# Kernel tuning notes

Hardware: AMD Instinct MI355X
Metric: run time of the kernel (lower is better)

## Reference

```python
import math
import jax, jax.numpy as jnp
import numpy as np

B, L, C, H = 2, 2048, 1024, 16
D = C // H


def new_gelu(x):
    return 0.5 * x * (1.0 + jnp.tanh(math.sqrt(2.0 / math.pi) * (x + 0.044715 * x ** 3)))


def layer_norm(x, w, b, eps=1e-5):
    mu = jnp.mean(x, axis=-1, keepdims=True)
    var = jnp.var(x, axis=-1, keepdims=True)
    return (x - mu) * jax.lax.rsqrt(var + eps) * w + b


def setup_inputs() -> dict:
    key = jax.random.key(0)
    ks = jax.random.split(key, 8)
    s = 0.02
    return {
        "x": jax.random.normal(ks[0], (B, L, C), dtype=jnp.float32),
        "ln1_w": jnp.ones((C,), jnp.float32),
        "ln1_b": jnp.zeros((C,), jnp.float32),
        "w_attn": jax.random.normal(ks[1], (C, 3 * C), dtype=jnp.float32) * s,
        "b_attn": jnp.zeros((3 * C,), jnp.float32),
        "w_proj": jax.random.normal(ks[2], (C, C), dtype=jnp.float32) * s,
        "b_proj": jnp.zeros((C,), jnp.float32),
        "ln2_w": jnp.ones((C,), jnp.float32),
        "ln2_b": jnp.zeros((C,), jnp.float32),
        "w_fc": jax.random.normal(ks[3], (C, 4 * C), dtype=jnp.float32) * s,
        "b_fc": jnp.zeros((4 * C,), jnp.float32),
        "w_fc2": jax.random.normal(ks[4], (4 * C, C), dtype=jnp.float32) * s,
        "b_fc2": jnp.zeros((C,), jnp.float32),
    }


def reference(x, ln1_w, ln1_b, w_attn, b_attn, w_proj, b_proj,
              ln2_w, ln2_b, w_fc, b_fc, w_fc2, b_fc2):
    # --- self-attention sublayer (pre-LN) ---
    h = layer_norm(x, ln1_w, ln1_b)
    qkv = h @ w_attn + b_attn                              # [B, L, 3C]
    q, k, v = jnp.split(qkv, 3, axis=-1)
    q = q.reshape(B, L, H, D)
    k = k.reshape(B, L, H, D)
    v = v.reshape(B, L, H, D)
    att = jnp.einsum("bqhd,bkhd->bhqk", q, k) * (1.0 / math.sqrt(D))
    causal = jnp.tril(jnp.ones((L, L), dtype=bool))
    att = jnp.where(causal[None, None], att, -jnp.inf)
    att = jax.nn.softmax(att, axis=-1)
    y = jnp.einsum("bhqk,bkhd->bqhd", att, v).reshape(B, L, C)
    y = y @ w_proj + b_proj
    x = x + y
    # --- MLP sublayer (pre-LN) ---
    h = layer_norm(x, ln2_w, ln2_b)
    h = new_gelu(h @ w_fc + b_fc)
    h = h @ w_fc2 + b_fc2
    return x + h
```

## Files before the change

### kernel.cpp

```cpp
#include <hip/hip_runtime.h>
#include <math.h>

#define B_ 2
#define L_ 2048
#define C_ 1024
#define H_ 16
#define M_ (B_*L_)

typedef short s16x8 __attribute__((ext_vector_type(8)));
typedef float f32x4 __attribute__((ext_vector_type(4)));

__device__ __forceinline__ unsigned short f2bf(float f) {
    unsigned int u = __float_as_uint(f);
    u += 0x7fffu + ((u >> 16) & 1u);
    return (unsigned short)(u >> 16);
}

__device__ __forceinline__ float fexp2(float x) {
#if __has_builtin(__builtin_amdgcn_exp2f)
    return __builtin_amdgcn_exp2f(x);
#else
    return exp2f(x);
#endif
}

__device__ __forceinline__ float frcp(float x) {
#if __has_builtin(__builtin_amdgcn_rcpf)
    return __builtin_amdgcn_rcpf(x);
#else
    return 1.0f / x;
#endif
}

__device__ __forceinline__ void gl_lds16(const void* g, void* l) {
    __builtin_amdgcn_global_load_lds(
        (const __attribute__((address_space(1))) void*)g,
        (__attribute__((address_space(3))) void*)l, 16, 0, 0);
}

#define VMCNT8() asm volatile("s_waitcnt vmcnt(8)" ::: "memory")
#define VMCNT6() asm volatile("s_waitcnt vmcnt(6)" ::: "memory")
#define VMCNT0() asm volatile("s_waitcnt vmcnt(0)" ::: "memory")
#define LGKM0()  asm volatile("s_waitcnt lgkmcnt(0)" ::: "memory")
#define SCHED0() __builtin_amdgcn_sched_barrier(0)

__device__ __forceinline__ void ln_row(const float* __restrict__ x,
                                       const float* __restrict__ w,
                                       const float* __restrict__ b,
                                       unsigned short* __restrict__ out,
                                       int row, int t,
                                       float* red0, float* red1, float* mv) {
    float4 v = ((const float4*)(x + (size_t)row * C_))[t];
    float s  = v.x + v.y + v.z + v.w;
    float s2 = v.x*v.x + v.y*v.y + v.z*v.z + v.w*v.w;
    #pragma unroll
    for (int off = 32; off > 0; off >>= 1) {
        s  += __shfl_down(s, off);
        s2 += __shfl_down(s2, off);
    }
    int wave = t >> 6, lane = t & 63;
    if (lane == 0) { red0[wave] = s; red1[wave] = s2; }
    __syncthreads();
    if (t == 0) {
        float a = red0[0] + red0[1] + red0[2] + red0[3];
        float c = red1[0] + red1[1] + red1[2] + red1[3];
        float mean = a * (1.0f / C_);
        mv[0] = mean;
        mv[1] = rsqrtf(c * (1.0f / C_) - mean * mean + 1e-5f);
    }
    __syncthreads();
    float mean = mv[0], rstd = mv[1];
    float4 wv = ((const float4*)w)[t];
    float4 bv = ((const float4*)b)[t];
    ushort4 o;
    o.x = f2bf((v.x - mean) * rstd * wv.x + bv.x);
    o.y = f2bf((v.y - mean) * rstd * wv.y + bv.y);
    o.z = f2bf((v.z - mean) * rstd * wv.z + bv.z);
    o.w = f2bf((v.w - mean) * rstd * wv.w + bv.w);
    *(ushort4*)&out[(size_t)row * C_ + t * 4] = o;
}

__global__ __launch_bounds__(256) void ln_bf16(const float* __restrict__ x,
                                               const float* __restrict__ w,
                                               const float* __restrict__ b,
                                               unsigned short* __restrict__ out) {
    __shared__ float red0[4], red1[4], mv[2];
    ln_row(x, w, b, out, blockIdx.x, threadIdx.x, red0, red1, mv);
}

__global__ __launch_bounds__(256) void prep_kernel(
    const float* __restrict__ W0, unsigned short* __restrict__ T0,
    const float* __restrict__ W1, unsigned short* __restrict__ T1,
    const float* __restrict__ W2, unsigned short* __restrict__ T2,
    const float* __restrict__ W3, unsigned short* __restrict__ T3,
    const float* __restrict__ x, const float* __restrict__ lnw,
    const float* __restrict__ lnb, unsigned short* __restrict__ h) {
    __shared__ unsigned short Ts[32][33];
    __shared__ float red0[4], red1[4], mv[2];
    int id = blockIdx.x;
    int t = threadIdx.x;
    if (id >= 12288) {
        ln_row(x, lnw, lnb, h, id - 12288, t, red0, red1, mv);
        return;
    }
    const float* W; unsigned short* WT; int R, C, bx, by;
    if (id < 3072)      { W = W0; WT = T0; R = 1024; C = 3072; bx = id % 96;  by = id / 96; }
    else if (id < 4096) { W = W1; WT = T1; R = 1024; C = 1024; id -= 3072; bx = id & 31;  by = id >> 5; }
    else if (id < 8192) { W = W2; WT = T2; R = 1024; C = 4096; id -= 4096; bx = id & 127; by = id >> 7; }
    else                { W = W3; WT = T3; R = 4096; C = 1024; id -= 8192; bx = id & 31;  by = id >> 5; }
    int tx = t & 31, ty = t >> 5;
    int c0 = bx * 32, r0 = by * 32;
    #pragma unroll
    for (int k = 0; k < 4; ++k)
        Ts[ty + 8*k][tx] = f2bf(W[(size_t)(r0 + ty + 8*k) * C + c0 + tx]);
    __syncthreads();
    #pragma unroll
    for (int k = 0; k < 4; ++k)
        WT[(size_t)(c0 + ty + 8*k) * R + r0 + tx] = Ts[tx][ty + 8*k];
}

__device__ __forceinline__ float gelu_f(float x) {
    float u2 = 1.5957691216057308f * (x + 0.044715f * x * x * x);
    return x * frcp(1.0f + __expf(-u2));
}

template<int ACT, int OBF, int TN, int SC, int KS, int VT, int XS>
__global__ __launch_bounds__(256) void bgemm(const unsigned short* __restrict__ A,
                                             const unsigned short* __restrict__ BT,
                                             const float* __restrict__ bias,
                                             const float* __restrict__ res,
                                             void* __restrict__ Cout,
                                             unsigned short* __restrict__ VtP,
                                             int M, int N, int K) {
    __shared__ __align__(16) unsigned short As[128 * 64];
    __shared__ __align__(16) unsigned short Bs[TN * 64];
    const int t = threadIdx.x, w = t >> 6, quad = (t & 63) >> 4, ln15 = t & 15;
    constexpr int FJ = TN / 32;
    const int woff_m = (w >> 1) * 64, woff_n = (w & 1) * (TN / 2);
    int bxi = blockIdx.x, byi = blockIdx.y;
    if (XS) {
        int id = bxi + (int)gridDim.x * byi;
        int nt = (int)gridDim.x, xcd = id & 7, loc = id >> 3;
        int per = (nt + 7) >> 3;
        bxi = xcd * per + (loc % per);
        byi = loc / per;
        if (bxi >= nt) { bxi = id % nt; byi = id / nt; }
    }
    const int m0g = byi * 128, n0g = bxi * TN;
    f32x4 acc[4][FJ];
    #pragma unroll
    for (int fi = 0; fi < 4; ++fi)
        #pragma unroll
        for (int fj = 0; fj < FJ; ++fj)
            #pragma unroll
            for (int i = 0; i < 4; ++i) acc[fi][fj][i] = 0.0f;

    const int kbeg = (KS > 1) ? (int)blockIdx.z * (K / KS) : 0;
    const int kiters = ((KS > 1) ? K / KS : K) >> 6;

    const unsigned short* ap[4];
    #pragma unroll
    for (int j = 0; j < 4; ++j) {
        int c = j * 256 + t, row = c >> 3, u = (c & 7) ^ (row & 7);
        ap[j] = A + (size_t)(m0g + row) * K + kbeg + u * 8;
    }
    const unsigned short* bp[FJ];
    #pragma unroll
    for (int j = 0; j < FJ; ++j) {
        int c = j * 256 + t, row = c >> 3, u = (c & 7) ^ (row & 7);
        bp[j] = BT + (size_t)(n0g + row) * K + kbeg + u * 8;
    }

    for (int kk = 0; kk < kiters; ++kk) {
        __syncthreads();
        #pragma unroll
        for (int j = 0; j < 4; ++j) {
            gl_lds16(ap[j], As + (j * 256 + w * 64) * 8);
            ap[j] += 64;
        }
        #pragma unroll
        for (int j = 0; j < FJ; ++j) {
            gl_lds16(bp[j], Bs + (j * 256 + w * 64) * 8);
            bp[j] += 64;
        }
        __syncthreads();
        #pragma unroll
        for (int s = 0; s < 2; ++s) {
            s16x8 af[4], bfr[FJ];
            #pragma unroll
            for (int f = 0; f < 4; ++f) {
                int row = woff_m + f * 16 + ln15;
                af[f] = *(const s16x8*)&As[(row * 8 + ((s * 4 + quad) ^ (row & 7))) * 8];
            }
            #pragma unroll
            for (int f = 0; f < FJ; ++f) {
                int row = woff_n + f * 16 + ln15;
                bfr[f] = *(const s16x8*)&Bs[(row * 8 + ((s * 4 + quad) ^ (row & 7))) * 8];
            }
            #pragma unroll
            for (int fi = 0; fi < 4; ++fi)
                #pragma unroll
                for (int fj = 0; fj < FJ; ++fj)
                    acc[fi][fj] = __builtin_amdgcn_mfma_f32_16x16x32_bf16(af[fi], bfr[fj], acc[fi][fj], 0, 0, 0);
        }
    }

    const int colb = n0g + woff_n + ln15;
    if (KS > 1) {
        float* P = (float*)Cout + (size_t)blockIdx.z * M * N;
        #pragma unroll
        for (int fj = 0; fj < FJ; ++fj) {
            const int col = colb + fj * 16;
            #pragma unroll
            for (int fi = 0; fi < 4; ++fi) {
                const int row0 = m0g + woff_m + fi * 16 + quad * 4;
                #pragma unroll
                for (int i = 0; i < 4; ++i)
                    P[(size_t)(row0 + i) * N + col] = acc[fi][fj][i];
            }
        }
        return;
    }
    #pragma unroll
    for (int fj = 0; fj < FJ; ++fj) {
        const int col = colb + fj * 16;
        const float bv = bias[col];
        const float sc = (SC && col < C_) ? 0.18033688011112042f : 1.0f;
        if (VT && col >= 2 * C_) {
            const int vcol = col - 2 * C_;
            #pragma unroll
            for (int fi = 0; fi < 4; ++fi) {
                const int row0 = m0g + woff_m + fi * 16 + quad * 4;
                const int bb = row0 >> 11, l = row0 & (L_ - 1);
                ushort4 pk;
                pk.x = f2bf(acc[fi][fj][0] + bv);
                pk.y = f2bf(acc[fi][fj][1] + bv);
                pk.z = f2bf(acc[fi][fj][2] + bv);
                pk.w = f2bf(acc[fi][fj][3] + bv);
                *(ushort4*)&VtP[(size_t)(bb * 1024 + vcol) * L_ + l] = pk;
            }
        } else {
            #pragma unroll
            for (int fi = 0; fi < 4; ++fi) {
                const int row0 = m0g + woff_m + fi * 16 + quad * 4;
                #pragma unroll
                for (int i = 0; i < 4; ++i) {
                    float v = acc[fi][fj][i] + bv;
                    if (ACT) v = gelu_f(v);
                    if (SC) v *= sc;
                    size_t off = (size_t)(row0 + i) * N + col;
                    if (res != nullptr) v += res[off];
                    if (OBF) ((unsigned short*)Cout)[off] = f2bf(v);
                    else     ((float*)Cout)[off] = v;
                }
            }
        }
    }
}

template<int ACT, int OBF, int BM, int SC, int KS, int VT, int XS>
__global__ __launch_bounds__(512) void bgemm2(const unsigned short* __restrict__ A,
                                              const unsigned short* __restrict__ BT,
                                              const float* __restrict__ bias,
                                              const float* __restrict__ res,
                                              void* __restrict__ Cout,
                                              unsigned short* __restrict__ VtP,
                                              int M, int N, int K) {
    constexpr int MR = BM / 32;
    constexpr int NR = 4;
    constexpr int WM = BM / 2;
    constexpr int RA = BM / 64;
    constexpr int RB = 4;
    __shared__ __align__(16) unsigned short As[2 * BM * 64];
    __shared__ __align__(16) unsigned short Bs[2 * 256 * 64];
    const int t = threadIdx.x, wv = t >> 6, quad = (t & 63) >> 4, ln15 = t & 15;
    const int wm = wv >> 2, wn = wv & 3;
    int bxi = blockIdx.x, byi = blockIdx.y, bzi = blockIdx.z;
    if (XS == 1) {
        int id = bxi + (int)gridDim.x * byi;
        int nt = (int)gridDim.x, xcd = id & 7, loc = id >> 3;
        int per = nt >> 3;
        bxi = xcd * per + (loc % per);
        byi = loc / per;
    } else if (XS == 2) {
        int gx = (int)gridDim.x;
        int id = bxi + gx * byi + (int)(gridDim.x * gridDim.y) * bzi;
        int xcd = id & 7;
        bxi = xcd % gx;
        bzi = xcd / gx;
        byi = id >> 3;
    }
    const int m0g = byi * BM, n0g = bxi * 256;

    f32x4 acc[MR][NR];
    #pragma unroll
    for (int mr = 0; mr < MR; ++mr)
        #pragma unroll
        for (int nr = 0; nr < NR; ++nr)
            #pragma unroll
            for (int i = 0; i < 4; ++i) acc[mr][nr][i] = 0.0f;

    const int kbeg = (KS > 1) ? bzi * (K / KS) : 0;
    const int NT = ((KS > 1) ? K / KS : K) >> 6;

    const unsigned short* ap[RA];
    #pragma unroll
    for (int j = 0; j < RA; ++j) {
        int c = j * 512 + t, row = c >> 3, u = (t & 7) ^ (row & 7);
        ap[j] = A + (size_t)(m0g + row) * K + kbeg + u * 8;
    }
    const unsigned short* bp[RB];
    #pragma unroll
    for (int j = 0; j < RB; ++j) {
        int c = j * 512 + t, row = c >> 3, u = (t & 7) ^ (row & 7);
        bp[j] = BT + (size_t)(n0g + row) * K + kbeg + u * 8;
    }

    auto STAGE = [&](int kt, int buf) {
        unsigned short* Ad = As + buf * (BM * 64);
        unsigned short* Bd = Bs + buf * (256 * 64);
        #pragma unroll
        for (int j = 0; j < RA; ++j)
            gl_lds16(ap[j] + (size_t)kt * 64, Ad + (j * 512 + wv * 64) * 8);
        #pragma unroll
        for (int j = 0; j < RB; ++j)
            gl_lds16(bp[j] + (size_t)kt * 64, Bd + (j * 512 + wv * 64) * 8);
    };

    STAGE(0, 0);
    STAGE(1, 1);
    if constexpr (RA + RB == 8) VMCNT8(); else VMCNT6();
    __builtin_amdgcn_s_barrier();

    int buf = 0;
    for (int kt = 0; kt < NT; ++kt) {
        const unsigned short* Ab = As + buf * (BM * 64);
        const unsigned short* Bb = Bs + buf * (256 * 64);
        s16x8 a0[MR], b0[NR], a1[MR], b1[NR];
        #pragma unroll
        for (int mr = 0; mr < MR; ++mr) {
            int row = wm * WM + mr * 16 + ln15;
            a0[mr] = *(const s16x8*)&Ab[(row * 8 + (quad ^ (row & 7))) * 8];
        }
        #pragma unroll
        for (int nr = 0; nr < NR; ++nr) {
            int row = wn * 64 + nr * 16 + ln15;
            b0[nr] = *(const s16x8*)&Bb[(row * 8 + (quad ^ (row & 7))) * 8];
        }
        #pragma unroll
        for (int mr = 0; mr < MR; ++mr)
            #pragma unroll
            for (int nr = 0; nr < NR; ++nr)
                acc[mr][nr] = __builtin_amdgcn_mfma_f32_16x16x32_bf16(a0[mr], b0[nr], acc[mr][nr], 0, 0, 0);
        #pragma unroll
        for (int mr = 0; mr < MR; ++mr) {
            int row = wm * WM + mr * 16 + ln15;
            a1[mr] = *(const s16x8*)&Ab[(row * 8 + ((4 + quad) ^ (row & 7))) * 8];
        }
        #pragma unroll
        for (int nr = 0; nr < NR; ++nr) {
            int row = wn * 64 + nr * 16 + ln15;
            b1[nr] = *(const s16x8*)&Bb[(row * 8 + ((4 + quad) ^ (row & 7))) * 8];
        }
        LGKM0();
        __builtin_amdgcn_sched_barrier(0);
        __builtin_amdgcn_s_barrier();
        if (kt + 2 < NT) STAGE(kt + 2, buf);
        __builtin_amdgcn_s_setprio(1);
        #pragma unroll
        for (int mr = 0; mr < MR; ++mr)
            #pragma unroll
            for (int nr = 0; nr < NR; ++nr)
                acc[mr][nr] = __builtin_amdgcn_mfma_f32_16x16x32_bf16(a1[mr], b1[nr], acc[mr][nr], 0, 0, 0);
        __builtin_amdgcn_s_setprio(0);
        if (kt + 2 < NT) {
            if constexpr (RA + RB == 8) VMCNT8(); else VMCNT6();
            __builtin_amdgcn_s_barrier();
        } else if (kt + 1 < NT) {
            VMCNT0();
            __builtin_amdgcn_s_barrier();
        }
        buf ^= 1;
    }

    const int colb = n0g + wn * 64 + ln15;
    if (KS > 1) {
        float* P = (float*)Cout + (size_t)bzi * M * N;
        #pragma unroll
        for (int nr = 0; nr < NR; ++nr) {
            const int col = colb + nr * 16;
            #pragma unroll
            for (int mr = 0; mr < MR; ++mr) {
                const int row0 = m0g + wm * WM + mr * 16 + quad * 4;
                #pragma unroll
                for (int i = 0; i < 4; ++i)
                    P[(size_t)(row0 + i) * N + col] = acc[mr][nr][i];
            }
        }
        return;
    }
    if constexpr (OBF && !VT && BM == 256) {
        if (res == nullptr) {
            unsigned short* Ep = As;
            unsigned short* Cg = (unsigned short*)Cout;
            #pragma unroll
            for (int half = 0; half < 2; ++half) {
                LGKM0(); __builtin_amdgcn_s_barrier();
                if (wm == half) {
                    #pragma unroll
                    for (int mr = 0; mr < MR; ++mr) {
                        #pragma unroll
                        for (int nr = 0; nr < NR; ++nr) {
                            const int col = wn * 64 + nr * 16 + ln15;
                            const float bv = bias[n0g + col];
                            #pragma unroll
                            for (int i = 0; i < 4; ++i) {
                                const int row = mr * 16 + quad * 4 + i;
                                float v = acc[mr][nr][i] + bv;
                                if (ACT) v = gelu_f(v);
                                if (SC && (n0g + col) < C_) v *= 0.18033688011112042f;
                                Ep[row * 256 + (col ^ (((row >> 2) & 3) << 4))] = f2bf(v);
                            }
                        }
                    }
                }
                LGKM0(); __builtin_amdgcn_s_barrier();
                #pragma unroll
                for (int it = 0; it < 8; ++it) {
                    int off = it * 4096 + t * 8;
                    int row = off >> 8, c0 = off & 255;
                    int sc0 = c0 ^ (((row >> 2) & 3) << 4);
                    s16x8 vld = *(const s16x8*)&Ep[row * 256 + sc0];
                    *(s16x8*)&Cg[(size_t)(m0g + half * 128 + row) * N + n0g + c0] = vld;
                }
            }
            return;
        }
    }
    #pragma unroll
    for (int nr = 0; nr < NR; ++nr) {
        const int col = colb + nr * 16;
        const float bv = bias[col];
        const float sc = (SC && col < C_) ? 0.18033688011112042f : 1.0f;
        if (VT && col >= 2 * C_) {
            const int vcol = col - 2 * C_;
            #pragma unroll
            for (int mr = 0; mr < MR; ++mr) {
                const int row0 = m0g + wm * WM + mr * 16 + quad * 4;
                const int bb = row0 >> 11, l = row0 & (L_ - 1);
                ushort4 pk;
                pk.x = f2bf(acc[mr][nr][0] + bv);
                pk.y = f2bf(acc[mr][nr][1] + bv);
                pk.z = f2bf(acc[mr][nr][2] + bv);
                pk.w = f2bf(acc[mr][nr][3] + bv);
                *(ushort4*)&VtP[(size_t)(bb * 1024 + vcol) * L_ + l] = pk;
            }
        } else {
            #pragma unroll
            for (int mr = 0; mr < MR; ++mr) {
                const int row0 = m0g + wm * WM + mr * 16 + quad * 4;
                #pragma unroll
                for (int i = 0; i < 4; ++i) {
                    float v = acc[mr][nr][i] + bv;
                    if (ACT) v = gelu_f(v);
                    if (SC) v *= sc;
                    size_t off = (size_t)(row0 + i) * N + col;
                    if (res != nullptr) v += res[off];
                    if (OBF) ((unsigned short*)Cout)[off] = f2bf(v);
                    else     ((float*)Cout)[off] = v;
                }
            }
        }
    }
}

__global__ __launch_bounds__(256) void combine_out(const float* __restrict__ p,
                                                   const float* __restrict__ bias,
                                                   const float* __restrict__ res,
                                                   float* __restrict__ out) {
    int idx = blockIdx.x * 256 + threadIdx.x;
    size_t off = (size_t)idx * 4;
    float4 a = *(const float4*)&p[off];
    float4 b = *(const float4*)&p[(size_t)M_ * C_ + off];
    float4 r = *(const float4*)&res[off];
    float4 bb = *(const float4*)&bias[off & (C_ - 1)];
    float4 o;
    o.x = a.x + b.x + r.x + bb.x;
    o.y = a.y + b.y + r.y + bb.y;
    o.z = a.z + b.z + r.z + bb.z;
    o.w = a.w + b.w + r.w + bb.w;
    *(float4*)&out[off] = o;
}

__global__ __launch_bounds__(256) void attn_kernel(const unsigned short* __restrict__ qkv,
                                                   const unsigned short* __restrict__ Vt,
                                                   unsigned short* __restrict__ y) {
    __shared__ __align__(16) unsigned short Qs[64 * 64];
    __shared__ __align__(16) unsigned short Ks[2 * 128 * 64];
    __shared__ __align__(16) unsigned short Vs[2 * 64 * 128];
    const int t = threadIdx.x, w = t >> 6, quad = (t & 63) >> 4, ln15 = t & 15;
    const int wq = w >> 1, wk = w & 1;
    const int id = blockIdx.x;
    const int bh = (id & 7) * 4 + ((id >> 3) & 3);
    const int qpair = id >> 5;
    const int b = bh >> 4, h = bh & 15;

    #pragma unroll 1
    for (int rep = 0; rep < 2; ++rep) {
        const int qt = rep == 0 ? (31 - qpair) : qpair;
        const int q0 = qt * 64;
        if (rep) __syncthreads();
        #pragma unroll
        for (int j = 0; j < 2; ++j) {
            int c = j * 256 + t;
            int row = c >> 3, u = (c & 7) ^ (row & 7);
            gl_lds16(qkv + (size_t)(b * L_ + q0 + row) * (3*C_) + h * 64 + u * 8,
                     Qs + (j * 256 + w * 64) * 8);
        }
        #pragma unroll
        for (int j = 0; j < 4; ++j) {
            int c = j * 256 + t;
            int row = c >> 3, u = (c & 7) ^ (row & 7);
            gl_lds16(qkv + (size_t)(b * L_ + row) * (3*C_) + C_ + h * 64 + u * 8,
                     Ks + (j * 256 + w * 64) * 8);
        }
        #pragma unroll
        for (int j = 0; j < 4; ++j) {
            int c = j * 256 + t;
            int row = c >> 4, u = (c & 15) ^ (row & 15);
            gl_lds16(Vt + (size_t)(bh * 64 + row) * L_ + u * 8,
                     Vs + (j * 256 + w * 64) * 8);
        }
        __syncthreads();

        s16x8 qb[2][2];
        #pragma unroll
        for (int qf = 0; qf < 2; ++qf) {
            int row = wq * 32 + qf * 16 + ln15;
            #pragma unroll
            for (int s = 0; s < 2; ++s)
                qb[qf][s] = *(const s16x8*)&Qs[row * 64 + (((s * 4 + quad)) ^ (row & 7)) * 8];
        }

        f32x4 O[4][2];
        float m_[2] = {-INFINITY, -INFINITY}, l_[2] = {0.0f, 0.0f};
        #pragma unroll
        for (int df = 0; df < 4; ++df)
            #pragma unroll
            for (int qf = 0; qf < 2; ++qf)
                #pragma unroll
                for (int i = 0; i < 4; ++i) O[df][qf][i] = 0.0f;

        const int nkt = (qt >> 1) + 1;
        int buf = 0;
        for (int kt = 0; kt < nkt; ++kt) {
            unsigned short* Kb = Ks + buf * (128 * 64);
            unsigned short* Vb = Vs + buf * (64 * 128);
            unsigned short* Kn = Ks + (buf ^ 1) * (128 * 64);
            unsigned short* Vn = Vs + (buf ^ 1) * (64 * 128);
            if (kt + 1 < nkt) {
                #pragma unroll
                for (int j = 0; j < 4; ++j) {
                    int c = j * 256 + t;
                    int row = c >> 3, u = (c & 7) ^ (row & 7);
                    gl_lds16(qkv + (size_t)(b * L_ + (kt + 1) * 128 + row) * (3*C_) + C_ + h * 64 + u * 8,
                             Kn + (j * 256 + w * 64) * 8);
                }
                #pragma unroll
                for (int j = 0; j < 4; ++j) {
                    int c = j * 256 + t;
                    int row = c >> 4, u = (c & 15) ^ (row & 15);
                    gl_lds16(Vt + (size_t)(bh * 64 + row) * L_ + (kt + 1) * 128 + u * 8,
                             Vn + (j * 256 + w * 64) * 8);
                }
            }

            f32x4 St[2][4];
            #pragma unroll
            for (int qf = 0; qf < 2; ++qf)
                #pragma unroll
                for (int kf = 0; kf < 4; ++kf)
                    #pragma unroll
                    for (int i = 0; i < 4; ++i) St[qf][kf][i] = 0.0f;
            #pragma unroll
            for (int s = 0; s < 2; ++s) {
                s16x8 ka[4];
                #pragma unroll
                for (int kf = 0; kf < 4; ++kf) {
                    int row = wk * 64 + kf * 16 + ln15;
                    ka[kf] = *(const s16x8*)&Kb[row * 64 + ((s * 4 + quad) ^ (row & 7)) * 8];
                }
                #pragma unroll
                for (int qf = 0; qf < 2; ++qf)
                    #pragma unroll
                    for (int kf = 0; kf < 4; ++kf)
                        St[qf][kf] = __builtin_amdgcn_mfma_f32_16x16x32_bf16(ka[kf], qb[qf][s], St[qf][kf], 0, 0, 0);
            }
            LGKM0(); SCHED0();
            __builtin_amdgcn_s_barrier();
            SCHED0();

            unsigned short* Pw = Kb + w * 2048;
            const bool diag = (kt == nkt - 1);
            #pragma unroll
            for (int qf = 0; qf < 2; ++qf) {
                const int qg = q0 + wq * 32 + qf * 16 + ln15;
                float mt = -INFINITY;
                if (diag) {
                    #pragma unroll
                    for (int kf = 0; kf < 4; ++kf)
                        #pragma unroll
                        for (int i = 0; i < 4; ++i) {
                            int key = kt * 128 + wk * 64 + kf * 16 + quad * 4 + i;
                            float sv = St[qf][kf][i];
                            sv = (key > qg) ? -INFINITY : sv;
                            St[qf][kf][i] = sv;
                            mt = fmaxf(mt, sv);
                        }
                } else {
                    #pragma unroll
                    for (int kf = 0; kf < 4; ++kf)
                        #pragma unroll
                        for (int i = 0; i < 4; ++i) mt = fmaxf(mt, St[qf][kf][i]);
                }
                mt = fmaxf(mt, __shfl_xor(mt, 16));
                mt = fmaxf(mt, __shfl_xor(mt, 32));
                const float mn = fmaxf(m_[qf], mt);
                const float ms = (mn == -INFINITY) ? 0.0f : mn;
                const float alpha = fexp2(m_[qf] - ms);
                float rs = 0.0f;
                #pragma unroll
                for (int kf = 0; kf < 4; ++kf)
                    #pragma unroll
                    for (int i = 0; i < 4; ++i) {
                        float e = fexp2(St[qf][kf][i] - ms);
                        St[qf][kf][i] = e;
                        rs += e;
                    }
                rs += __shfl_xor(rs, 16);
                rs += __shfl_xor(rs, 32);
                l_[qf] = l_[qf] * alpha + rs;
                m_[qf] = mn;
                #pragma unroll
                for (int df = 0; df < 4; ++df) O[df][qf] *= alpha;
                #pragma unroll
                for (int kf = 0; kf < 4; ++kf) {
                    int row = qf * 16 + ln15;
                    int slot = (kf * 2 + (quad >> 1)) ^ (row & 7);
                    unsigned u0 = __float_as_uint(St[qf][kf][0]) + 0x8000u;
                    unsigned u1 = __float_as_uint(St[qf][kf][1]) + 0x8000u;
                    unsigned u2 = __float_as_uint(St[qf][kf][2]) + 0x8000u;
                    unsigned u3 = __float_as_uint(St[qf][kf][3]) + 0x8000u;
                    uint2 pk;
                    pk.x = __builtin_amdgcn_perm(u1, u0, 0x07060302u);
                    pk.y = __builtin_amdgcn_perm(u3, u2, 0x07060302u);
                    *(uint2*)&Pw[row * 64 + slot * 8 + (quad & 1) * 4] = pk;
                }
            }

            #pragma unroll
            for (int s2 = 0; s2 < 2; ++s2) {
                s16x8 pb[2], va[4];
                #pragma unroll
                for (int qf = 0; qf < 2; ++qf) {
                    int row = qf * 16 + ln15;
                    pb[qf] = *(const s16x8*)&Pw[row * 64 + ((s2 * 4 + quad) ^ (row & 7)) * 8];
                }
                #pragma unroll
                for (int df = 0; df < 4; ++df) {
                    int row = df * 16 + ln15;
                    int uu = wk * 8 + s2 * 4 + quad;
                    va[df] = *(const s16x8*)&Vb[row * 128 + (uu ^ (row & 15)) * 8];
                }
                #pragma unroll
                for (int df = 0; df < 4; ++df)
                    #pragma unroll
                    for (int qf = 0; qf < 2; ++qf)
                        O[df][qf] = __builtin_amdgcn_mfma_f32_16x16x32_bf16(va[df], pb[qf], O[df][qf], 0, 0, 0);
            }

            if (kt + 1 < nkt) {
                LGKM0(); VMCNT0(); SCHED0();
                __builtin_amdgcn_s_barrier();
                SCHED0();
            }
            buf ^= 1;
        }

        __syncthreads();
        float* OB  = (float*)Ks;
        float* MLm = (float*)Qs;
        float* MLl = MLm + 64;
        if (wk == 1) {
            #pragma unroll
            for (int qf = 0; qf < 2; ++qf) {
                int rq = wq * 32 + qf * 16 + ln15;
                if (quad == 0) { MLm[rq] = m_[qf]; MLl[rq] = l_[qf]; }
                #pragma unroll
                for (int df = 0; df < 4; ++df) {
                    float4 o;
                    o.x = O[df][qf][0]; o.y = O[df][qf][1]; o.z = O[df][qf][2]; o.w = O[df][qf][3];
                    *(float4*)&OB[rq * 64 + (((df * 4 + quad) ^ (rq & 15)) << 2)] = o;
                }
            }
        }
        __syncthreads();
        if (wk == 0) {
            #pragma unroll
            for (int qf = 0; qf < 2; ++qf) {
                const int rq = wq * 32 + qf * 16 + ln15;
                const float m1 = MLm[rq], l1 = MLl[rq];
                const float mF = fmaxf(m_[qf], m1);
                float e0 = fexp2(m_[qf] - mF);
                float e1 = (m1 == -INFINITY) ? 0.0f : fexp2(m1 - mF);
                const float linv = frcp(l_[qf] * e0 + l1 * e1);
                e0 *= linv; e1 *= linv;
                #pragma unroll
                for (int df = 0; df < 4; ++df) {
                    float4 o1 = *(const float4*)&OB[rq * 64 + (((df * 4 + quad) ^ (rq & 15)) << 2)];
                    ushort4 yv;
                    yv.x = f2bf(O[df][qf][0] * e0 + o1.x * e1);
                    yv.y = f2bf(O[df][qf][1] * e0 + o1.y * e1);
                    yv.z = f2bf(O[df][qf][2] * e0 + o1.z * e1);
                    yv.w = f2bf(O[df][qf][3] * e0 + o1.w * e1);
                    *(ushort4*)&y[(size_t)(b * L_ + q0 + rq) * C_ + h * 64 + df * 16 + quad * 4] = yv;
                }
            }
        }
    }
}

#define MB(x) ((size_t)(x) << 20)

extern "C" void kernel_launch(void* const* d_in, const int* in_sizes, int n_in,
                              void* d_out, int out_size, void* d_ws, size_t ws_size,
                              hipStream_t stream) {
    const float* x      = (const float*)d_in[0];
    const float* ln1_w  = (const float*)d_in[1];
    const float* ln1_b  = (const float*)d_in[2];
    const float* w_attn = (const float*)d_in[3];
    const float* b_attn = (const float*)d_in[4];
    const float* w_proj = (const float*)d_in[5];
    const float* b_proj = (const float*)d_in[6];
    const float* ln2_w  = (const float*)d_in[7];
    const float* ln2_b  = (const float*)d_in[8];
    const float* w_fc   = (const float*)d_in[9];
    const float* b_fc   = (const float*)d_in[10];
    const float* w_fc2  = (const float*)d_in[11];
    const float* b_fc2  = (const float*)d_in[12];
    float* out = (float*)d_out;

    char* ws = (char*)d_ws;
    unsigned short* wT1  = (unsigned short*)(ws + MB(0));
    unsigned short* wT2  = (unsigned short*)(ws + MB(6));
    unsigned short* wT3  = (unsigned short*)(ws + MB(8));
    unsigned short* wT4  = (unsigned short*)(ws + MB(16));
    unsigned short* h_bf = (unsigned short*)(ws + MB(24));
    unsigned short* qkv  = (unsigned short*)(ws + MB(32));
    unsigned short* Vt   = (unsigned short*)(ws + MB(56));
    unsigned short* y_bf = (unsigned short*)(ws + MB(64));
    float*          x1   = (float*)(ws + MB(72));
    unsigned short* f_bf = (unsigned short*)(ws + MB(88));
    float*          part = (float*)(ws + MB(32));
    dim3 b256(256), b512(512);

    prep_kernel<<<12288 + M_, b256, 0, stream>>>(w_attn, wT1, w_proj, wT2,
                                                 w_fc, wT3, w_fc2, wT4,
                                                 x, ln1_w, ln1_b, h_bf);
    bgemm<0,1,128,1,1,1,0><<<dim3(3*C_/128, M_/128), b256, 0, stream>>>(
        h_bf, wT1, b_attn, nullptr, qkv, Vt, M_, 3*C_, C_);
    attn_kernel<<<512, b256, 0, stream>>>(qkv, Vt, y_bf);
    bgemm<0,0,64,0,1,0,0><<<dim3(C_/64, M_/128), b256, 0, stream>>>(
        y_bf, wT2, b_proj, x, x1, nullptr, M_, C_, C_);
    ln_bf16<<<M_, b256, 0, stream>>>(x1, ln2_w, ln2_b, h_bf);
    bgemm2<1,1,256,0,1,0,1><<<dim3(4*C_/256, M_/256), b512, 0, stream>>>(
        h_bf, wT3, b_fc, nullptr, f_bf, nullptr, M_, 4*C_, C_);
    bgemm2<0,0,128,0,2,0,2><<<dim3(C_/256, M_/128, 2), b512, 0, stream>>>(
        f_bf, wT4, nullptr, nullptr, part, nullptr, M_, C_, 4*C_);
    combine_out<<<(M_*C_)/(4*256), b256, 0, stream>>>(part, b_fc2, x1, out);
}
```

Baseline: 333.2 us.

## Interleave GEMM MFMA halves with LDS reads and add lazy softmax rescaling

The GEMM main loop now splits each k-step's MFMA block into two halves over the N fragments. The first half is issued between the LDS fragment loads, with extra barriers and priority raises, so matrix math overlaps shared-memory reads. Separately, the flash-attention softmax skips the running-max update and the rescaling of O and l whenever the new tile max stays within 8 (log2 units) of the current max for every lane. This saves exp and multiply work. The lazy threshold lets exponentials reach up to 2^8 before renormalisation, and the extra barriers add synchronisation cost.

```diff
diff --git a/kernel.cpp b/kernel.cpp
--- a/kernel.cpp
+++ b/kernel.cpp
@@ -347,11 +347,16 @@
             int row = wn * 64 + nr * 16 + ln15;
             b0[nr] = *(const s16x8*)&Bb[(row * 8 + (quad ^ (row & 7))) * 8];
         }
+        __builtin_amdgcn_s_barrier();
+        LGKM0(); SCHED0();
+        __builtin_amdgcn_s_setprio(1);
         #pragma unroll
         for (int mr = 0; mr < MR; ++mr)
             #pragma unroll
-            for (int nr = 0; nr < NR; ++nr)
+            for (int nr = 0; nr < 2; ++nr)
                 acc[mr][nr] = __builtin_amdgcn_mfma_f32_16x16x32_bf16(a0[mr], b0[nr], acc[mr][nr], 0, 0, 0);
+        __builtin_amdgcn_s_setprio(0);
+        __builtin_amdgcn_s_barrier();
         #pragma unroll
         for (int mr = 0; mr < MR; ++mr) {
             int row = wm * WM + mr * 16 + ln15;
@@ -362,15 +367,29 @@
             int row = wn * 64 + nr * 16 + ln15;
             b1[nr] = *(const s16x8*)&Bb[(row * 8 + ((4 + quad) ^ (row & 7))) * 8];
         }
-        LGKM0();
-        __builtin_amdgcn_sched_barrier(0);
+        __builtin_amdgcn_s_setprio(1);
+        #pragma unroll
+        for (int mr = 0; mr < MR; ++mr)
+            #pragma unroll
+            for (int nr = 2; nr < 4; ++nr)
+                acc[mr][nr] = __builtin_amdgcn_mfma_f32_16x16x32_bf16(a0[mr], b0[nr], acc[mr][nr], 0, 0, 0);
+        __builtin_amdgcn_s_setprio(0);
+        LGKM0(); SCHED0();
         __builtin_amdgcn_s_barrier();
         if (kt + 2 < NT) STAGE(kt + 2, buf);
         __builtin_amdgcn_s_setprio(1);
         #pragma unroll
         for (int mr = 0; mr < MR; ++mr)
             #pragma unroll
-            for (int nr = 0; nr < NR; ++nr)
+            for (int nr = 0; nr < 2; ++nr)
+                acc[mr][nr] = __builtin_amdgcn_mfma_f32_16x16x32_bf16(a1[mr], b1[nr], acc[mr][nr], 0, 0, 0);
+        __builtin_amdgcn_s_setprio(0);
+        __builtin_amdgcn_s_barrier();
+        __builtin_amdgcn_s_setprio(1);
+        #pragma unroll
+        for (int mr = 0; mr < MR; ++mr)
+            #pragma unroll
+            for (int nr = 2; nr < 4; ++nr)
                 acc[mr][nr] = __builtin_amdgcn_mfma_f32_16x16x32_bf16(a1[mr], b1[nr], acc[mr][nr], 0, 0, 0);
         __builtin_amdgcn_s_setprio(0);
         if (kt + 2 < NT) {
@@ -625,9 +644,18 @@
                 }
                 mt = fmaxf(mt, __shfl_xor(mt, 16));
                 mt = fmaxf(mt, __shfl_xor(mt, 32));
-                const float mn = fmaxf(m_[qf], mt);
-                const float ms = (mn == -INFINITY) ? 0.0f : mn;
-                const float alpha = fexp2(m_[qf] - ms);
+                float ms;
+                if (__all(mt <= m_[qf] + 8.0f && m_[qf] > -INFINITY)) {
+                    ms = m_[qf];
+                } else {
+                    const float mn = fmaxf(m_[qf], mt);
+                    ms = (mn == -INFINITY) ? 0.0f : mn;
+                    const float alpha = fexp2(m_[qf] - ms);
+                    l_[qf] *= alpha;
+                    m_[qf] = mn;
+                    #pragma unroll
+                    for (int df = 0; df < 4; ++df) O[df][qf] *= alpha;
+                }
                 float rs = 0.0f;
                 #pragma unroll
                 for (int kf = 0; kf < 4; ++kf)
@@ -639,10 +667,7 @@
                     }
                 rs += __shfl_xor(rs, 16);
                 rs += __shfl_xor(rs, 32);
-                l_[qf] = l_[qf] * alpha + rs;
-                m_[qf] = mn;
-                #pragma unroll
-                for (int df = 0; df < 4; ++df) O[df][qf] *= alpha;
+                l_[qf] += rs;
                 #pragma unroll
                 for (int kf = 0; kf < 4; ++kf) {
                     int row = qf * 16 + ln15;
```

Result: slower. 347.9 us (+4.4%).

## Replace split-K FC2 with 128x128 tiles and skip softmax rescaling

Applied to the files above, without the earlier changes.

Adds a BN template parameter to bgemm2 so FC2 can run with 128x128 tiles and no split-K. Bias and residual are then fused into the GEMM epilogue, which removes the partial-sum buffer and the combine_out kernel. Separately, the attention softmax keeps the stale running max when every new block max is within 8 (log2 units) of it, skipping the alpha rescale of O and l. That threshold relies on fp32 headroom for exponents up to 2^8. The FC2 grid becomes 256 blocks of 512 threads with a longer K loop per block, which may lower occupancy compared with the split-K version.

```diff
diff --git a/kernel.cpp b/kernel.cpp
--- a/kernel.cpp
+++ b/kernel.cpp
@@ -40,6 +40,7 @@
 
 #define VMCNT8() asm volatile("s_waitcnt vmcnt(8)" ::: "memory")
 #define VMCNT6() asm volatile("s_waitcnt vmcnt(6)" ::: "memory")
+#define VMCNT4() asm volatile("s_waitcnt vmcnt(4)" ::: "memory")
 #define VMCNT0() asm volatile("s_waitcnt vmcnt(0)" ::: "memory")
 #define LGKM0()  asm volatile("s_waitcnt lgkmcnt(0)" ::: "memory")
 #define SCHED0() __builtin_amdgcn_sched_barrier(0)
@@ -258,7 +259,7 @@
     }
 }
 
-template<int ACT, int OBF, int BM, int SC, int KS, int VT, int XS>
+template<int ACT, int OBF, int BM, int BN, int SC, int KS, int VT, int XS>
 __global__ __launch_bounds__(512) void bgemm2(const unsigned short* __restrict__ A,
                                               const unsigned short* __restrict__ BT,
                                               const float* __restrict__ bias,
@@ -267,12 +268,12 @@
                                               unsigned short* __restrict__ VtP,
                                               int M, int N, int K) {
     constexpr int MR = BM / 32;
-    constexpr int NR = 4;
+    constexpr int NR = BN / 64;
     constexpr int WM = BM / 2;
     constexpr int RA = BM / 64;
-    constexpr int RB = 4;
+    constexpr int RB = BN / 64;
     __shared__ __align__(16) unsigned short As[2 * BM * 64];
-    __shared__ __align__(16) unsigned short Bs[2 * 256 * 64];
+    __shared__ __align__(16) unsigned short Bs[2 * BN * 64];
     const int t = threadIdx.x, wv = t >> 6, quad = (t & 63) >> 4, ln15 = t & 15;
     const int wm = wv >> 2, wn = wv & 3;
     int bxi = blockIdx.x, byi = blockIdx.y, bzi = blockIdx.z;
@@ -290,7 +291,7 @@
         bzi = xcd / gx;
         byi = id >> 3;
     }
-    const int m0g = byi * BM, n0g = bxi * 256;
+    const int m0g = byi * BM, n0g = bxi * BN;
 
     f32x4 acc[MR][NR];
     #pragma unroll
@@ -318,7 +319,7 @@
 
     auto STAGE = [&](int kt, int buf) {
         unsigned short* Ad = As + buf * (BM * 64);
-        unsigned short* Bd = Bs + buf * (256 * 64);
+        unsigned short* Bd = Bs + buf * (BN * 64);
         #pragma unroll
         for (int j = 0; j < RA; ++j)
             gl_lds16(ap[j] + (size_t)kt * 64, Ad + (j * 512 + wv * 64) * 8);
@@ -329,13 +330,15 @@
 
     STAGE(0, 0);
     STAGE(1, 1);
-    if constexpr (RA + RB == 8) VMCNT8(); else VMCNT6();
+    if constexpr (RA + RB == 8) VMCNT8();
+    else if constexpr (RA + RB == 6) VMCNT6();
+    else VMCNT4();
     __builtin_amdgcn_s_barrier();
 
     int buf = 0;
     for (int kt = 0; kt < NT; ++kt) {
         const unsigned short* Ab = As + buf * (BM * 64);
-        const unsigned short* Bb = Bs + buf * (256 * 64);
+        const unsigned short* Bb = Bs + buf * (BN * 64);
         s16x8 a0[MR], b0[NR], a1[MR], b1[NR];
         #pragma unroll
         for (int mr = 0; mr < MR; ++mr) {
@@ -344,7 +347,7 @@
         }
         #pragma unroll
         for (int nr = 0; nr < NR; ++nr) {
-            int row = wn * 64 + nr * 16 + ln15;
+            int row = wn * (NR * 16) + nr * 16 + ln15;
             b0[nr] = *(const s16x8*)&Bb[(row * 8 + (quad ^ (row & 7))) * 8];
         }
         #pragma unroll
@@ -359,7 +362,7 @@
         }
         #pragma unroll
         for (int nr = 0; nr < NR; ++nr) {
-            int row = wn * 64 + nr * 16 + ln15;
+            int row = wn * (NR * 16) + nr * 16 + ln15;
             b1[nr] = *(const s16x8*)&Bb[(row * 8 + ((4 + quad) ^ (row & 7))) * 8];
         }
         LGKM0();
@@ -374,7 +377,9 @@
                 acc[mr][nr] = __builtin_amdgcn_mfma_f32_16x16x32_bf16(a1[mr], b1[nr], acc[mr][nr], 0, 0, 0);
         __builtin_amdgcn_s_setprio(0);
         if (kt + 2 < NT) {
-            if constexpr (RA + RB == 8) VMCNT8(); else VMCNT6();
+            if constexpr (RA + RB == 8) VMCNT8();
+            else if constexpr (RA + RB == 6) VMCNT6();
+            else VMCNT4();
             __builtin_amdgcn_s_barrier();
         } else if (kt + 1 < NT) {
             VMCNT0();
@@ -383,7 +388,7 @@
         buf ^= 1;
     }
 
-    const int colb = n0g + wn * 64 + ln15;
+    const int colb = n0g + wn * (NR * 16) + ln15;
     if (KS > 1) {
         float* P = (float*)Cout + (size_t)bzi * M * N;
         #pragma unroll
@@ -399,7 +404,7 @@
         }
         return;
     }
-    if constexpr (OBF && !VT && BM == 256) {
+    if constexpr (OBF && !VT && BM == 256 && BN == 256) {
         if (res == nullptr) {
             unsigned short* Ep = As;
             unsigned short* Cg = (unsigned short*)Cout;
@@ -474,24 +479,6 @@
     }
 }
 
-__global__ __launch_bounds__(256) void combine_out(const float* __restrict__ p,
-                                                   const float* __restrict__ bias,
-                                                   const float* __restrict__ res,
-                                                   float* __restrict__ out) {
-    int idx = blockIdx.x * 256 + threadIdx.x;
-    size_t off = (size_t)idx * 4;
-    float4 a = *(const float4*)&p[off];
-    float4 b = *(const float4*)&p[(size_t)M_ * C_ + off];
-    float4 r = *(const float4*)&res[off];
-    float4 bb = *(const float4*)&bias[off & (C_ - 1)];
-    float4 o;
-    o.x = a.x + b.x + r.x + bb.x;
-    o.y = a.y + b.y + r.y + bb.y;
-    o.z = a.z + b.z + r.z + bb.z;
-    o.w = a.w + b.w + r.w + bb.w;
-    *(float4*)&out[off] = o;
-}
-
 __global__ __launch_bounds__(256) void attn_kernel(const unsigned short* __restrict__ qkv,
                                                    const unsigned short* __restrict__ Vt,
                                                    unsigned short* __restrict__ y) {
@@ -625,9 +612,18 @@
                 }
                 mt = fmaxf(mt, __shfl_xor(mt, 16));
                 mt = fmaxf(mt, __shfl_xor(mt, 32));
-                const float mn = fmaxf(m_[qf], mt);
-                const float ms = (mn == -INFINITY) ? 0.0f : mn;
-                const float alpha = fexp2(m_[qf] - ms);
+                float ms;
+                if (__all(mt <= m_[qf] + 8.0f && m_[qf] > -INFINITY)) {
+                    ms = m_[qf];
+                } else {
+                    const float mn = fmaxf(m_[qf], mt);
+                    ms = (mn == -INFINITY) ? 0.0f : mn;
+                    const float alpha = fexp2(m_[qf] - ms);
+                    l_[qf] *= alpha;
+                    m_[qf] = mn;
+                    #pragma unroll
+                    for (int df = 0; df < 4; ++df) O[df][qf] *= alpha;
+                }
                 float rs = 0.0f;
                 #pragma unroll
                 for (int kf = 0; kf < 4; ++kf)
@@ -639,10 +635,7 @@
                     }
                 rs += __shfl_xor(rs, 16);
                 rs += __shfl_xor(rs, 32);
-                l_[qf] = l_[qf] * alpha + rs;
-                m_[qf] = mn;
-                #pragma unroll
-                for (int df = 0; df < 4; ++df) O[df][qf] *= alpha;
+                l_[qf] += rs;
                 #pragma unroll
                 for (int kf = 0; kf < 4; ++kf) {
                     int row = qf * 16 + ln15;
@@ -761,7 +754,6 @@
     unsigned short* y_bf = (unsigned short*)(ws + MB(64));
     float*          x1   = (float*)(ws + MB(72));
     unsigned short* f_bf = (unsigned short*)(ws + MB(88));
-    float*          part = (float*)(ws + MB(32));
     dim3 b256(256), b512(512);
 
     prep_kernel<<<12288 + M_, b256, 0, stream>>>(w_attn, wT1, w_proj, wT2,
@@ -773,9 +765,8 @@
     bgemm<0,0,64,0,1,0,0><<<dim3(C_/64, M_/128), b256, 0, stream>>>(
         y_bf, wT2, b_proj, x, x1, nullptr, M_, C_, C_);
     ln_bf16<<<M_, b256, 0, stream>>>(x1, ln2_w, ln2_b, h_bf);
-    bgemm2<1,1,256,0,1,0,1><<<dim3(4*C_/256, M_/256), b512, 0, stream>>>(
+    bgemm2<1,1,256,256,0,1,0,1><<<dim3(4*C_/256, M_/256), b512, 0, stream>>>(
         h_bf, wT3, b_fc, nullptr, f_bf, nullptr, M_, 4*C_, C_);
-    bgemm2<0,0,128,0,2,0,2><<<dim3(C_/256, M_/128, 2), b512, 0, stream>>>(
-        f_bf, wT4, nullptr, nullptr, part, nullptr, M_, C_, 4*C_);
-    combine_out<<<(M_*C_)/(4*256), b256, 0, stream>>>(part, b_fc2, x1, out);
-}
+    bgemm2<0,0,128,128,0,1,0,1><<<dim3(C_/128, M_/128), b512, 0, stream>>>(
+        f_bf, wT4, b_fc2, x1, out, nullptr, M_, C_, 4*C_);
+}
```

Result: slower. 351.4 us (+5.5%).
